# Performance work log

Measured on AMD Instinct MI355X. Metric: run time of the kernel, lower is better.

The kernel has to match this reference:

```python
import jax, jax.numpy as jnp
import numpy as np

NUM_HEADS = 4
HEAD_DIM = 16  # out_channels // num_heads = 64 // 4
IN_C = 64
OUT_C = 64


def setup_inputs() -> dict:
    key = jax.random.key(0)
    k1, k2, k3 = jax.random.split(key, 3)
    x = jax.random.normal(k1, (2, IN_C, 64, 64), dtype=jnp.float32)
    # nn.Linear(in_channels, 3*out_channels): weight (3*OUT_C, IN_C), bias (3*OUT_C,)
    s = 1.0 / np.sqrt(IN_C)
    qkv_w = jax.random.uniform(k2, (3 * OUT_C, IN_C), minval=-s, maxval=s, dtype=jnp.float32)
    qkv_b = jax.random.uniform(k3, (3 * OUT_C,), minval=-s, maxval=s, dtype=jnp.float32)
    return {"x": x, "qkv_w": qkv_w, "qkv_b": qkv_b}


def reference(x, qkv_w, qkv_b):
    B, C, H, W = x.shape
    N = H * W
    # (B,C,H,W) -> (B,N,C)
    tokens = x.reshape(B, C, N).transpose(0, 2, 1)
    qkv = tokens @ qkv_w.T + qkv_b  # (B,N,3*OUT_C)
    q, k, v = jnp.split(qkv, 3, axis=-1)
    def to_heads(t):
        return t.reshape(B, N, NUM_HEADS, HEAD_DIM).transpose(0, 2, 1, 3)  # (B,h,N,d)
    q, k, v = to_heads(q), to_heads(k), to_heads(v)
    scale = 1.0 / np.sqrt(HEAD_DIM)
    attn = jnp.einsum('bhnd,bhmd->bhnm', q, k) * scale  # (B,h,N,N)
    attn = jax.nn.softmax(attn, axis=-1)
    # dropout is identity in eval mode
    out = jnp.einsum('bhnm,bhmd->bhnd', attn, v)  # (B,h,N,d)
    out = out.transpose(0, 2, 1, 3).reshape(B, N, OUT_C)  # (B,N,outC)
    out = out.transpose(0, 2, 1).reshape(B, OUT_C, H, W)
    return out
```

## Files before the change

### kernel.cpp

```cpp
#include <hip/hip_runtime.h>
#include <hip/hip_bf16.h>


#define NTOK 4096
#define HD   16
#define BH   8
#define QUART 1024
#define PIT2 (QUART/32/2)
#define PITERS (QUART/32)

typedef __attribute__((ext_vector_type(4))) short short4v;
typedef __attribute__((ext_vector_type(4))) float float4v;
typedef __attribute__((ext_vector_type(4))) ushort ushort4v;
typedef __attribute__((ext_vector_type(2))) unsigned uint2v;

__device__ __forceinline__ ushort f2bf(float f) {
  unsigned u = __builtin_bit_cast(unsigned, f);
  u += 0x7fffu + ((u >> 16) & 1u);
  return (ushort)(u >> 16);
}

__device__ __forceinline__ float fast_exp2(float x) {
#if __has_builtin(__builtin_amdgcn_exp2f)
  return __builtin_amdgcn_exp2f(x);
#else
  return exp2f(x);
#endif
}

__device__ __forceinline__ short4v pack4_bf16(float a, float b, float c, float d) {
  __hip_bfloat162 lo = __float22bfloat162_rn(make_float2(a, b));
  __hip_bfloat162 hi = __float22bfloat162_rn(make_float2(c, d));
  unsigned ulo, uhi;
  __builtin_memcpy(&ulo, &lo, 4);
  __builtin_memcpy(&uhi, &hi, 4);
  uint2v u = { ulo, uhi };
  return __builtin_bit_cast(short4v, u);
}

#define QB_OFF 0
#define KB_OFF ((size_t)BH*NTOK*HD)
#define VT_OFF (2*(size_t)BH*NTOK*HD)

__global__ __launch_bounds__(192) void qkv_proj(
    const float* __restrict__ x, const float* __restrict__ w,
    const float* __restrict__ bias, ushort* __restrict__ wsu) {
  const int TOK = 8, TILES = 2;
  int blk = blockIdx.x;
  int b   = blk >> 8;
  int n00 = (blk & 255) * (TOK*TILES);
  int o   = threadIdx.x;

  float wr[64];
  const float4* w4 = reinterpret_cast<const float4*>(w + o*64);
  #pragma unroll
  for (int i = 0; i < 16; ++i) {
    float4 tt = w4[i];
    wr[4*i+0]=tt.x; wr[4*i+1]=tt.y; wr[4*i+2]=tt.z; wr[4*i+3]=tt.w;
  }
  float bb = bias[o];

  int part = o >> 6;
  int oo   = o & 63;
  int h    = oo >> 4;
  int dd   = oo & 15;
  int bh   = b*4 + h;
  const float QSCALE = 0.25f * 1.44269504f;

  ushort* Qt = wsu + QB_OFF;
  ushort* Kb = wsu + KB_OFF;
  ushort* Vf = wsu + VT_OFF;

  __shared__ float4 xs4[64][2];
  const float4* x4 = reinterpret_cast<const float4*>(x);

  #pragma unroll 1
  for (int tile = 0; tile < TILES; ++tile) {
    int n0 = n00 + tile*TOK;
    for (int idx = threadIdx.x; idx < 128; idx += 192) {
      int c = idx >> 1, t4 = idx & 1;
      xs4[c][t4] = x4[((size_t)b*64 + c)*(NTOK/4) + (n0 >> 2) + t4];
    }
    __syncthreads();

    #pragma unroll
    for (int t4 = 0; t4 < 2; ++t4) {
      float a[4] = {bb, bb, bb, bb};
      #pragma unroll
      for (int c = 0; c < 64; ++c) {
        float4 xv = xs4[c][t4];
        float wv = wr[c];
        a[0] = fmaf(xv.x, wv, a[0]);
        a[1] = fmaf(xv.y, wv, a[1]);
        a[2] = fmaf(xv.z, wv, a[2]);
        a[3] = fmaf(xv.w, wv, a[3]);
      }
      if (part == 0) {
        ushort4v vv = { f2bf(a[0]*QSCALE), f2bf(a[1]*QSCALE),
                        f2bf(a[2]*QSCALE), f2bf(a[3]*QSCALE) };
        *(ushort4v*)(Qt + ((size_t)bh*HD + dd)*NTOK + n0 + t4*4) = vv;
      } else if (part == 1) {
        #pragma unroll
        for (int j = 0; j < 4; ++j)
          Kb[((size_t)bh*NTOK + n0 + t4*4 + j)*HD + dd] = f2bf(a[j]);
      } else {
        int m = n0 + t4*4;
        size_t idx = (size_t)bh*NTOK*HD + (m >> 4)*256 + ((m & 15) >> 2)*64 + dd*4;
        ushort4v vv = { f2bf(a[0]), f2bf(a[1]), f2bf(a[2]), f2bf(a[3]) };
        *(ushort4v*)(Vf + idx) = vv;
      }
    }
    __syncthreads();
  }
}

__global__ __launch_bounds__(256, 4) void attn_mfma(
    const ushort* __restrict__ wsu, float* __restrict__ out) {
  const ushort* Qt = wsu + QB_OFF;
  const ushort* Kb = wsu + KB_OFF;
  const ushort* Vt = wsu + VT_OFF;

  int bh    = blockIdx.x >> 7;
  int qblk  = blockIdx.x & 127;
  int tid   = threadIdx.x;
  int quart = tid >> 6;
  int lane  = tid & 63;
  int lr    = lane & 15;
  int g4    = (lane >> 4) << 2;
  int qbase = qblk*32;

  __shared__ float comb[3][64][11];

  const ushort* Qh = Qt + (size_t)bh*HD*NTOK;
  const ushort* Kh = Kb + ((size_t)bh*NTOK + (size_t)quart*QUART)*HD;
  const ushort* Vh = Vt + (size_t)bh*NTOK*HD + (size_t)quart*QUART*HD;

  short4v qf0, qf1;
  #pragma unroll
  for (int j = 0; j < 4; ++j) {
    qf0[j] = (short)Qh[(size_t)(g4+j)*NTOK + qbase      + lr];
    qf1[j] = (short)Qh[(size_t)(g4+j)*NTOK + qbase + 16 + lr];
  }

  const ushort* kp = Kh + lr*HD + (lane >> 4)*4;
  const ushort* vp = Vh + lane*4;

  float4v a0e = {0.f,0.f,0.f,0.f}, a0o = {0.f,0.f,0.f,0.f};
  float4v a1e = {0.f,0.f,0.f,0.f}, a1o = {0.f,0.f,0.f,0.f};
  float l0 = 0.f, l1 = 0.f;

#define ITER(ke, ko, ve, vo)                                                \
  do {                                                                      \
    float4v zero = {0.f,0.f,0.f,0.f};                                       \
    __builtin_amdgcn_s_setprio(1);                                          \
    float4v s0e = __builtin_amdgcn_mfma_f32_16x16x16bf16_1k(ke, qf0, zero, 0,0,0); \
    float4v s0o = __builtin_amdgcn_mfma_f32_16x16x16bf16_1k(ko, qf0, zero, 0,0,0); \
    float4v s1e = __builtin_amdgcn_mfma_f32_16x16x16bf16_1k(ke, qf1, zero, 0,0,0); \
    float4v s1o = __builtin_amdgcn_mfma_f32_16x16x16bf16_1k(ko, qf1, zero, 0,0,0); \
    float p0e0 = fast_exp2(s0e[0]), p0e1 = fast_exp2(s0e[1]);               \
    float p0e2 = fast_exp2(s0e[2]), p0e3 = fast_exp2(s0e[3]);               \
    float p0o0 = fast_exp2(s0o[0]), p0o1 = fast_exp2(s0o[1]);               \
    float p0o2 = fast_exp2(s0o[2]), p0o3 = fast_exp2(s0o[3]);               \
    float p1e0 = fast_exp2(s1e[0]), p1e1 = fast_exp2(s1e[1]);               \
    float p1e2 = fast_exp2(s1e[2]), p1e3 = fast_exp2(s1e[3]);               \
    float p1o0 = fast_exp2(s1o[0]), p1o1 = fast_exp2(s1o[1]);               \
    float p1o2 = fast_exp2(s1o[2]), p1o3 = fast_exp2(s1o[3]);               \
    l0 += (p0e0 + p0e1) + (p0e2 + p0e3) + (p0o0 + p0o1) + (p0o2 + p0o3);    \
    l1 += (p1e0 + p1e1) + (p1e2 + p1e3) + (p1o0 + p1o1) + (p1o2 + p1o3);    \
    short4v pb0e = pack4_bf16(p0e0, p0e1, p0e2, p0e3);                      \
    short4v pb0o = pack4_bf16(p0o0, p0o1, p0o2, p0o3);                      \
    short4v pb1e = pack4_bf16(p1e0, p1e1, p1e2, p1e3);                      \
    short4v pb1o = pack4_bf16(p1o0, p1o1, p1o2, p1o3);                      \
    a0e = __builtin_amdgcn_mfma_f32_16x16x16bf16_1k(ve, pb0e, a0e, 0,0,0);  \
    a0o = __builtin_amdgcn_mfma_f32_16x16x16bf16_1k(vo, pb0o, a0o, 0,0,0);  \
    a1e = __builtin_amdgcn_mfma_f32_16x16x16bf16_1k(ve, pb1e, a1e, 0,0,0);  \
    a1o = __builtin_amdgcn_mfma_f32_16x16x16bf16_1k(vo, pb1o, a1o, 0,0,0);  \
    __builtin_amdgcn_s_setprio(0);                                          \
  } while (0)

  short4v kAe = *(const short4v*)(kp);
  short4v kAo = *(const short4v*)(kp + 256);
  short4v vAe = *(const short4v*)(vp);
  short4v vAo = *(const short4v*)(vp + 256);
  short4v kBe = *(const short4v*)(kp + 512);
  short4v kBo = *(const short4v*)(kp + 768);
  short4v vBe = *(const short4v*)(vp + 512);
  short4v vBo = *(const short4v*)(vp + 768);

  #pragma unroll 4
  for (int it2 = 0; it2 < PITERS/2; ++it2) {
    int oA = (2*it2 + 2) * 512;
    int oB = (2*it2 + 3) * 512;
    short4v nkAe = *(const short4v*)(kp + oA);
    short4v nkAo = *(const short4v*)(kp + oA + 256);
    short4v nvAe = *(const short4v*)(vp + oA);
    short4v nvAo = *(const short4v*)(vp + oA + 256);
    short4v nkBe = *(const short4v*)(kp + oB);
    short4v nkBo = *(const short4v*)(kp + oB + 256);
    short4v nvBe = *(const short4v*)(vp + oB);
    short4v nvBo = *(const short4v*)(vp + oB + 256);

    ITER(kAe, kAo, vAe, vAo);
    ITER(kBe, kBo, vBe, vBo);

    kAe = nkAe; kAo = nkAo; vAe = nvAe; vAo = nvAo;
    kBe = nkBe; kBo = nkBo; vBe = nvBe; vBo = nvBo;
  }
#undef ITER

  float o0[4], o1[4];
  #pragma unroll
  for (int r = 0; r < 4; ++r) {
    o0[r] = a0e[r] + a0o[r];
    o1[r] = a1e[r] + a1o[r];
  }

  if (quart != 0) {
    float* cp = &comb[quart-1][lane][0];
    cp[0] = o0[0]; cp[1] = o0[1]; cp[2] = o0[2]; cp[3] = o0[3];
    cp[4] = o1[0]; cp[5] = o1[1]; cp[6] = o1[2]; cp[7] = o1[3];
    cp[8] = l0;    cp[9] = l1;
  }
  __syncthreads();
  if (quart == 0) {
    #pragma unroll
    for (int wv = 0; wv < 3; ++wv) {
      const float* cp = &comb[wv][lane][0];
      o0[0] += cp[0]; o0[1] += cp[1]; o0[2] += cp[2]; o0[3] += cp[3];
      o1[0] += cp[4]; o1[1] += cp[5]; o1[2] += cp[6]; o1[3] += cp[7];
      l0 += cp[8];    l1 += cp[9];
    }
    l0 += __shfl_xor(l0, 16); l0 += __shfl_xor(l0, 32);
    l1 += __shfl_xor(l1, 16); l1 += __shfl_xor(l1, 32);
    float inv0 = 1.0f / l0, inv1 = 1.0f / l1;

    int b = bh >> 2, h = bh & 3;
    float* ob = out + ((size_t)(b*64 + h*16 + g4)) * NTOK;
    #pragma unroll
    for (int r = 0; r < 4; ++r) {
      ob[(size_t)r*NTOK + qbase      + lr] = o0[r] * inv0;
      ob[(size_t)r*NTOK + qbase + 16 + lr] = o1[r] * inv1;
    }
  }
}

extern "C" void kernel_launch(void* const* d_in, const int* in_sizes, int n_in,
                              void* d_out, int out_size, void* d_ws, size_t ws_size,
                              hipStream_t stream) {
  const float* x    = (const float*)d_in[0];
  const float* w    = (const float*)d_in[1];
  const float* bias = (const float*)d_in[2];
  float* out  = (float*)d_out;
  ushort* wsu = (ushort*)d_ws;

  qkv_proj <<<512,  192, 0, stream>>>(x, w, bias, wsu);
  attn_mfma<<<1024, 256, 0, stream>>>(wsu, out);
}
```

Measured before the change: 41.35 us.

## Process 64 queries per block across 8 waves to raise K/V reuse

Each attention block now covers 64 query rows, held as four 16-row tiles, instead of 32. The key range is split across 8 waves of 512 keys each instead of 4 waves of 1024. Every loaded K/V fragment feeds four query tiles rather than two, halving K/V load traffic per unit of compute, and the grid becomes 512 blocks of 512 threads. The cost is more accumulator registers per wave under a launch bound of 512 threads with 4 blocks per SM, which may force a tighter register limit or spills, plus a larger LDS reduction across 7 waves.

```diff
diff --git a/kernel.cpp b/kernel.cpp
--- a/kernel.cpp
+++ b/kernel.cpp
@@ -5,9 +5,8 @@
 #define NTOK 4096
 #define HD   16
 #define BH   8
-#define QUART 1024
-#define PIT2 (QUART/32/2)
-#define PITERS (QUART/32)
+#define EIGHTH 512
+#define PITERS (EIGHTH/32)
 
 typedef __attribute__((ext_vector_type(4))) short short4v;
 typedef __attribute__((ext_vector_type(4))) float float4v;
@@ -114,67 +113,64 @@
   }
 }
 
-__global__ __launch_bounds__(256, 4) void attn_mfma(
+__global__ __launch_bounds__(512, 4) void attn_mfma(
     const ushort* __restrict__ wsu, float* __restrict__ out) {
   const ushort* Qt = wsu + QB_OFF;
   const ushort* Kb = wsu + KB_OFF;
   const ushort* Vt = wsu + VT_OFF;
 
-  int bh    = blockIdx.x >> 7;
-  int qblk  = blockIdx.x & 127;
-  int tid   = threadIdx.x;
-  int quart = tid >> 6;
-  int lane  = tid & 63;
-  int lr    = lane & 15;
-  int g4    = (lane >> 4) << 2;
-  int qbase = qblk*32;
-
-  __shared__ float comb[3][64][11];
+  int bh   = blockIdx.x >> 6;
+  int qgrp = blockIdx.x & 63;
+  int tid  = threadIdx.x;
+  int wid  = tid >> 6;
+  int lane = tid & 63;
+  int lr   = lane & 15;
+  int g4   = (lane >> 4) << 2;
+  int qbase = qgrp*64;
+
+  __shared__ float comb[7][64][20];
 
   const ushort* Qh = Qt + (size_t)bh*HD*NTOK;
-  const ushort* Kh = Kb + ((size_t)bh*NTOK + (size_t)quart*QUART)*HD;
-  const ushort* Vh = Vt + (size_t)bh*NTOK*HD + (size_t)quart*QUART*HD;
-
-  short4v qf0, qf1;
+  const ushort* Kh = Kb + ((size_t)bh*NTOK + (size_t)wid*EIGHTH)*HD;
+  const ushort* Vh = Vt + (size_t)bh*NTOK*HD + (size_t)wid*EIGHTH*HD;
+
+  short4v qf[4];
   #pragma unroll
-  for (int j = 0; j < 4; ++j) {
-    qf0[j] = (short)Qh[(size_t)(g4+j)*NTOK + qbase      + lr];
-    qf1[j] = (short)Qh[(size_t)(g4+j)*NTOK + qbase + 16 + lr];
-  }
+  for (int qi = 0; qi < 4; ++qi)
+    #pragma unroll
+    for (int j = 0; j < 4; ++j)
+      qf[qi][j] = (short)Qh[(size_t)(g4+j)*NTOK + qbase + qi*16 + lr];
 
   const ushort* kp = Kh + lr*HD + (lane >> 4)*4;
   const ushort* vp = Vh + lane*4;
 
-  float4v a0e = {0.f,0.f,0.f,0.f}, a0o = {0.f,0.f,0.f,0.f};
-  float4v a1e = {0.f,0.f,0.f,0.f}, a1o = {0.f,0.f,0.f,0.f};
-  float l0 = 0.f, l1 = 0.f;
+  float4v ae[4], ao[4];
+  float lsum[4];
+  #pragma unroll
+  for (int qi = 0; qi < 4; ++qi) {
+    ae[qi] = (float4v){0.f,0.f,0.f,0.f};
+    ao[qi] = (float4v){0.f,0.f,0.f,0.f};
+    lsum[qi] = 0.f;
+  }
 
 #define ITER(ke, ko, ve, vo)                                                \
   do {                                                                      \
     float4v zero = {0.f,0.f,0.f,0.f};                                       \
     __builtin_amdgcn_s_setprio(1);                                          \
-    float4v s0e = __builtin_amdgcn_mfma_f32_16x16x16bf16_1k(ke, qf0, zero, 0,0,0); \
-    float4v s0o = __builtin_amdgcn_mfma_f32_16x16x16bf16_1k(ko, qf0, zero, 0,0,0); \
-    float4v s1e = __builtin_amdgcn_mfma_f32_16x16x16bf16_1k(ke, qf1, zero, 0,0,0); \
-    float4v s1o = __builtin_amdgcn_mfma_f32_16x16x16bf16_1k(ko, qf1, zero, 0,0,0); \
-    float p0e0 = fast_exp2(s0e[0]), p0e1 = fast_exp2(s0e[1]);               \
-    float p0e2 = fast_exp2(s0e[2]), p0e3 = fast_exp2(s0e[3]);               \
-    float p0o0 = fast_exp2(s0o[0]), p0o1 = fast_exp2(s0o[1]);               \
-    float p0o2 = fast_exp2(s0o[2]), p0o3 = fast_exp2(s0o[3]);               \
-    float p1e0 = fast_exp2(s1e[0]), p1e1 = fast_exp2(s1e[1]);               \
-    float p1e2 = fast_exp2(s1e[2]), p1e3 = fast_exp2(s1e[3]);               \
-    float p1o0 = fast_exp2(s1o[0]), p1o1 = fast_exp2(s1o[1]);               \
-    float p1o2 = fast_exp2(s1o[2]), p1o3 = fast_exp2(s1o[3]);               \
-    l0 += (p0e0 + p0e1) + (p0e2 + p0e3) + (p0o0 + p0o1) + (p0o2 + p0o3);    \
-    l1 += (p1e0 + p1e1) + (p1e2 + p1e3) + (p1o0 + p1o1) + (p1o2 + p1o3);    \
-    short4v pb0e = pack4_bf16(p0e0, p0e1, p0e2, p0e3);                      \
-    short4v pb0o = pack4_bf16(p0o0, p0o1, p0o2, p0o3);                      \
-    short4v pb1e = pack4_bf16(p1e0, p1e1, p1e2, p1e3);                      \
-    short4v pb1o = pack4_bf16(p1o0, p1o1, p1o2, p1o3);                      \
-    a0e = __builtin_amdgcn_mfma_f32_16x16x16bf16_1k(ve, pb0e, a0e, 0,0,0);  \
-    a0o = __builtin_amdgcn_mfma_f32_16x16x16bf16_1k(vo, pb0o, a0o, 0,0,0);  \
-    a1e = __builtin_amdgcn_mfma_f32_16x16x16bf16_1k(ve, pb1e, a1e, 0,0,0);  \
-    a1o = __builtin_amdgcn_mfma_f32_16x16x16bf16_1k(vo, pb1o, a1o, 0,0,0);  \
+    _Pragma("unroll")                                                       \
+    for (int qi = 0; qi < 4; ++qi) {                                        \
+      float4v se = __builtin_amdgcn_mfma_f32_16x16x16bf16_1k(ke, qf[qi], zero, 0,0,0); \
+      float4v so = __builtin_amdgcn_mfma_f32_16x16x16bf16_1k(ko, qf[qi], zero, 0,0,0); \
+      float pe0 = fast_exp2(se[0]), pe1 = fast_exp2(se[1]);                 \
+      float pe2 = fast_exp2(se[2]), pe3 = fast_exp2(se[3]);                 \
+      float po0 = fast_exp2(so[0]), po1 = fast_exp2(so[1]);                 \
+      float po2 = fast_exp2(so[2]), po3 = fast_exp2(so[3]);                 \
+      lsum[qi] += (pe0 + pe1) + (pe2 + pe3) + (po0 + po1) + (po2 + po3);    \
+      short4v pbe = pack4_bf16(pe0, pe1, pe2, pe3);                         \
+      short4v pbo = pack4_bf16(po0, po1, po2, po3);                         \
+      ae[qi] = __builtin_amdgcn_mfma_f32_16x16x16bf16_1k(ve, pbe, ae[qi], 0,0,0); \
+      ao[qi] = __builtin_amdgcn_mfma_f32_16x16x16bf16_1k(vo, pbo, ao[qi], 0,0,0); \
+    }                                                                       \
     __builtin_amdgcn_s_setprio(0);                                          \
   } while (0)
 
@@ -187,7 +183,7 @@
   short4v vBe = *(const short4v*)(vp + 512);
   short4v vBo = *(const short4v*)(vp + 768);
 
-  #pragma unroll 4
+  #pragma unroll 2
   for (int it2 = 0; it2 < PITERS/2; ++it2) {
     int oA = (2*it2 + 2) * 512;
     int oB = (2*it2 + 3) * 512;
@@ -208,38 +204,45 @@
   }
 #undef ITER
 
-  float o0[4], o1[4];
-  #pragma unroll
-  for (int r = 0; r < 4; ++r) {
-    o0[r] = a0e[r] + a0o[r];
-    o1[r] = a1e[r] + a1o[r];
-  }
-
-  if (quart != 0) {
-    float* cp = &comb[quart-1][lane][0];
-    cp[0] = o0[0]; cp[1] = o0[1]; cp[2] = o0[2]; cp[3] = o0[3];
-    cp[4] = o1[0]; cp[5] = o1[1]; cp[6] = o1[2]; cp[7] = o1[3];
-    cp[8] = l0;    cp[9] = l1;
+  if (wid != 0) {
+    float* cp = &comb[wid-1][lane][0];
+    #pragma unroll
+    for (int qi = 0; qi < 4; ++qi) {
+      #pragma unroll
+      for (int r = 0; r < 4; ++r)
+        cp[qi*4 + r] = ae[qi][r] + ao[qi][r];
+      cp[16 + qi] = lsum[qi];
+    }
   }
   __syncthreads();
-  if (quart == 0) {
-    #pragma unroll
-    for (int wv = 0; wv < 3; ++wv) {
+  if (wid == 0) {
+    float o4[4][4], lt[4];
+    #pragma unroll
+    for (int qi = 0; qi < 4; ++qi) {
+      #pragma unroll
+      for (int r = 0; r < 4; ++r) o4[qi][r] = ae[qi][r] + ao[qi][r];
+      lt[qi] = lsum[qi];
+    }
+    #pragma unroll
+    for (int wv = 0; wv < 7; ++wv) {
       const float* cp = &comb[wv][lane][0];
-      o0[0] += cp[0]; o0[1] += cp[1]; o0[2] += cp[2]; o0[3] += cp[3];
-      o1[0] += cp[4]; o1[1] += cp[5]; o1[2] += cp[6]; o1[3] += cp[7];
-      l0 += cp[8];    l1 += cp[9];
-    }
-    l0 += __shfl_xor(l0, 16); l0 += __shfl_xor(l0, 32);
-    l1 += __shfl_xor(l1, 16); l1 += __shfl_xor(l1, 32);
-    float inv0 = 1.0f / l0, inv1 = 1.0f / l1;
-
+      #pragma unroll
+      for (int qi = 0; qi < 4; ++qi) {
+        #pragma unroll
+        for (int r = 0; r < 4; ++r) o4[qi][r] += cp[qi*4 + r];
+        lt[qi] += cp[16 + qi];
+      }
+    }
     int b = bh >> 2, h = bh & 3;
     float* ob = out + ((size_t)(b*64 + h*16 + g4)) * NTOK;
     #pragma unroll
-    for (int r = 0; r < 4; ++r) {
-      ob[(size_t)r*NTOK + qbase      + lr] = o0[r] * inv0;
-      ob[(size_t)r*NTOK + qbase + 16 + lr] = o1[r] * inv1;
+    for (int qi = 0; qi < 4; ++qi) {
+      float l = lt[qi];
+      l += __shfl_xor(l, 16); l += __shfl_xor(l, 32);
+      float inv = 1.0f / l;
+      #pragma unroll
+      for (int r = 0; r < 4; ++r)
+        ob[(size_t)r*NTOK + qbase + qi*16 + lr] = o4[qi][r] * inv;
     }
   }
 }
@@ -253,6 +256,6 @@
   float* out  = (float*)d_out;
   ushort* wsu = (ushort*)d_ws;
 
-  qkv_proj <<<512,  192, 0, stream>>>(x, w, bias, wsu);
-  attn_mfma<<<1024, 256, 0, stream>>>(wsu, out);
-}
+  qkv_proj <<<512, 192, 0, stream>>>(x, w, bias, wsu);
+  attn_mfma<<<512, 512, 0, stream>>>(wsu, out);
+}
```

Result: slower. 45.79 us (+10.7%).

## Restructure QKV projection to token-per-lane and store Q token-major

Applied to the files above, without the earlier changes.

The projection kernel now assigns one token per lane and one (part, head) pair per wavefront. Each lane holds the 64 input channels in registers and reads weights as wave-uniform loads, replacing the shared-memory tile loop and its barriers. Q is stored token-major, like K, so the attention kernel can load each Q fragment with one vector load instead of four strided scalar loads. The V stores are now scattered 2-byte writes, and keeping 64 floats of x per lane raises register pressure.

```diff
diff --git a/kernel.cpp b/kernel.cpp
--- a/kernel.cpp
+++ b/kernel.cpp
@@ -6,7 +6,6 @@
 #define HD   16
 #define BH   8
 #define QUART 1024
-#define PIT2 (QUART/32/2)
 #define PITERS (QUART/32)
 
 typedef __attribute__((ext_vector_type(4))) short short4v;
@@ -42,75 +41,68 @@
 #define KB_OFF ((size_t)BH*NTOK*HD)
 #define VT_OFF (2*(size_t)BH*NTOK*HD)
 
-__global__ __launch_bounds__(192) void qkv_proj(
+__global__ __launch_bounds__(256) void qkv_proj(
     const float* __restrict__ x, const float* __restrict__ w,
     const float* __restrict__ bias, ushort* __restrict__ wsu) {
-  const int TOK = 8, TILES = 2;
-  int blk = blockIdx.x;
-  int b   = blk >> 8;
-  int n00 = (blk & 255) * (TOK*TILES);
-  int o   = threadIdx.x;
-
-  float wr[64];
-  const float4* w4 = reinterpret_cast<const float4*>(w + o*64);
-  #pragma unroll
-  for (int i = 0; i < 16; ++i) {
-    float4 tt = w4[i];
-    wr[4*i+0]=tt.x; wr[4*i+1]=tt.y; wr[4*i+2]=tt.z; wr[4*i+3]=tt.w;
-  }
-  float bb = bias[o];
-
-  int part = o >> 6;
-  int oo   = o & 63;
-  int h    = oo >> 4;
-  int dd   = oo & 15;
+  int tg   = blockIdx.x / 3;
+  int cg   = blockIdx.x % 3;
+  int wid  = threadIdx.x >> 6;
+  int lane = threadIdx.x & 63;
+  int combo = cg*4 + wid;
+  int part = combo >> 2;
+  int h    = combo & 3;
+  int b    = tg >> 6;
+  int np   = (tg & 63)*64 + lane;
   int bh   = b*4 + h;
   const float QSCALE = 0.25f * 1.44269504f;
 
-  ushort* Qt = wsu + QB_OFF;
+  float xr[64];
+  const float* xp = x + (size_t)b*64*NTOK + np;
+  #pragma unroll
+  for (int c = 0; c < 64; ++c)
+    xr[c] = xp[(size_t)c*NTOK];
+
+  const float* wp = w + (size_t)(part*64 + h*16)*64;
+  const float* bp = bias + part*64 + h*16;
+
+  unsigned res[8];
+
+  #pragma unroll
+  for (int oo = 0; oo < 16; ++oo) {
+    const float4* w4 = reinterpret_cast<const float4*>(wp + oo*64);
+    float acc = bp[oo];
+    #pragma unroll
+    for (int i = 0; i < 16; ++i) {
+      float4 wv = w4[i];
+      acc = fmaf(xr[4*i+0], wv.x, acc);
+      acc = fmaf(xr[4*i+1], wv.y, acc);
+      acc = fmaf(xr[4*i+2], wv.z, acc);
+      acc = fmaf(xr[4*i+3], wv.w, acc);
+    }
+    float val = (part == 0) ? acc*QSCALE : acc;
+    unsigned u = f2bf(val);
+    if ((oo & 1) == 0) res[oo >> 1] = u;
+    else               res[oo >> 1] |= (u << 16);
+  }
+
+  ushort* Qb = wsu + QB_OFF;
   ushort* Kb = wsu + KB_OFF;
   ushort* Vf = wsu + VT_OFF;
 
-  __shared__ float4 xs4[64][2];
-  const float4* x4 = reinterpret_cast<const float4*>(x);
-
-  #pragma unroll 1
-  for (int tile = 0; tile < TILES; ++tile) {
-    int n0 = n00 + tile*TOK;
-    for (int idx = threadIdx.x; idx < 128; idx += 192) {
-      int c = idx >> 1, t4 = idx & 1;
-      xs4[c][t4] = x4[((size_t)b*64 + c)*(NTOK/4) + (n0 >> 2) + t4];
-    }
-    __syncthreads();
-
-    #pragma unroll
-    for (int t4 = 0; t4 < 2; ++t4) {
-      float a[4] = {bb, bb, bb, bb};
-      #pragma unroll
-      for (int c = 0; c < 64; ++c) {
-        float4 xv = xs4[c][t4];
-        float wv = wr[c];
-        a[0] = fmaf(xv.x, wv, a[0]);
-        a[1] = fmaf(xv.y, wv, a[1]);
-        a[2] = fmaf(xv.z, wv, a[2]);
-        a[3] = fmaf(xv.w, wv, a[3]);
-      }
-      if (part == 0) {
-        ushort4v vv = { f2bf(a[0]*QSCALE), f2bf(a[1]*QSCALE),
-                        f2bf(a[2]*QSCALE), f2bf(a[3]*QSCALE) };
-        *(ushort4v*)(Qt + ((size_t)bh*HD + dd)*NTOK + n0 + t4*4) = vv;
-      } else if (part == 1) {
-        #pragma unroll
-        for (int j = 0; j < 4; ++j)
-          Kb[((size_t)bh*NTOK + n0 + t4*4 + j)*HD + dd] = f2bf(a[j]);
-      } else {
-        int m = n0 + t4*4;
-        size_t idx = (size_t)bh*NTOK*HD + (m >> 4)*256 + ((m & 15) >> 2)*64 + dd*4;
-        ushort4v vv = { f2bf(a[0]), f2bf(a[1]), f2bf(a[2]), f2bf(a[3]) };
-        *(ushort4v*)(Vf + idx) = vv;
-      }
-    }
-    __syncthreads();
+  if (part == 0) {
+    uint4* dst = (uint4*)(Qb + ((size_t)bh*NTOK + np)*HD);
+    dst[0] = make_uint4(res[0], res[1], res[2], res[3]);
+    dst[1] = make_uint4(res[4], res[5], res[6], res[7]);
+  } else if (part == 1) {
+    uint4* dst = (uint4*)(Kb + ((size_t)bh*NTOK + np)*HD);
+    dst[0] = make_uint4(res[0], res[1], res[2], res[3]);
+    dst[1] = make_uint4(res[4], res[5], res[6], res[7]);
+  } else {
+    ushort* vb = Vf + (size_t)bh*NTOK*HD
+               + (np >> 4)*256 + ((np & 15) >> 2)*64 + (np & 3);
+    #pragma unroll
+    for (int d = 0; d < 16; ++d)
+      vb[d*4] = (ushort)(res[d >> 1] >> ((d & 1)*16));
   }
 }
 
@@ -131,16 +123,12 @@
 
   __shared__ float comb[3][64][11];
 
-  const ushort* Qh = Qt + (size_t)bh*HD*NTOK;
+  const ushort* Qh = Qt + (size_t)bh*NTOK*HD;
   const ushort* Kh = Kb + ((size_t)bh*NTOK + (size_t)quart*QUART)*HD;
   const ushort* Vh = Vt + (size_t)bh*NTOK*HD + (size_t)quart*QUART*HD;
 
-  short4v qf0, qf1;
-  #pragma unroll
-  for (int j = 0; j < 4; ++j) {
-    qf0[j] = (short)Qh[(size_t)(g4+j)*NTOK + qbase      + lr];
-    qf1[j] = (short)Qh[(size_t)(g4+j)*NTOK + qbase + 16 + lr];
-  }
+  short4v qf0 = *(const short4v*)(Qh + (size_t)(qbase      + lr)*HD + g4);
+  short4v qf1 = *(const short4v*)(Qh + (size_t)(qbase + 16 + lr)*HD + g4);
 
   const ushort* kp = Kh + lr*HD + (lane >> 4)*4;
   const ushort* vp = Vh + lane*4;
@@ -253,6 +241,6 @@
   float* out  = (float*)d_out;
   ushort* wsu = (ushort*)d_ws;
 
-  qkv_proj <<<512,  192, 0, stream>>>(x, w, bias, wsu);
+  qkv_proj <<<384,  256, 0, stream>>>(x, w, bias, wsu);
   attn_mfma<<<1024, 256, 0, stream>>>(wsu, out);
 }
```

Result: slower. 49.66 us (+20.1%).
